# Kernel optimization log

Measured on AMD Instinct MI355X. Metric: run time of the kernel, lower is better.

## Reference

```python
import jax, jax.numpy as jnp
import numpy as np

RESOLUTION = 64
EPS = 1e-08


def setup_inputs() -> dict:
    key = jax.random.key(0)
    k1, k2 = jax.random.split(key)
    pts = jax.random.uniform(k1, (8, 3, 65536), dtype=jnp.float32)
    feat = jax.random.normal(k2, (8, 32, 65536), dtype=jnp.float32)
    return {"pts": pts, "feat": feat}


def reference(pts, feat):
    R = RESOLUTION
    B, _, N = pts.shape
    C = feat.shape[1]
    # Voxel index computation is done under no_grad in the original.
    p = jax.lax.stop_gradient(pts)
    p = p - jnp.min(p, axis=2, keepdims=True)  # per-sample, per-axis min shift
    # Global scalar max of per-point L2 norms (over all batches & points).
    norm_max = jnp.max(jnp.linalg.norm(p, axis=1))
    p = p / (norm_max + EPS)
    idx3 = (p * (R - 1)).astype(jnp.int32)  # [B, 3, N], floor via truncation (coords >= 0)
    vox = idx3[:, 0] + idx3[:, 1] * R + idx3[:, 2] * (R * R)  # [B, N] flat voxel ids

    featT = jnp.transpose(feat, (0, 2, 1))  # [B, N, C]

    def per_sample(v, f):
        # scatter-mean of point features into R^3 voxels; empty voxels -> 0
        sums = jax.ops.segment_sum(f, v, num_segments=R ** 3)          # [R^3, C]
        cnt = jax.ops.segment_sum(jnp.ones((v.shape[0],), f.dtype), v,
                                  num_segments=R ** 3)                 # [R^3]
        return sums / jnp.maximum(cnt, 1.0)[:, None]

    voxel = jax.vmap(per_sample)(vox, featT)  # [B, R^3, C]
    return jnp.transpose(voxel, (0, 2, 1)).reshape(B, C, R, R, R)
```

## Files before the change

kernel.cpp:

```cpp
#include <hip/hip_runtime.h>

#define RES 64
#define R3  (RES*RES*RES)
#define BB  8
#define CC  32
#define NN  65536
#define NBINS (BB*R3)
#define NPTS  (BB*NN)
#define NORM_EPS 1e-8f

#define SCAN_BLK 1024
#define NBLK (NBINS/SCAN_BLK)

#define OFF_COUNTS  4096
#define OFF_OFFSETS (OFF_COUNTS  + NBINS*4)
#define OFF_TOTALS  (OFF_OFFSETS + NBINS*4)
#define OFF_VOX     (OFF_TOTALS  + 65536)
#define OFF_ORDER   (OFF_VOX     + NPTS*4)
#define OFF_FEATT   (OFF_ORDER   + NPTS*4)

__global__ __launch_bounds__(1024) void k_min(const float* __restrict__ pts, float* __restrict__ mins) {
    int ba = blockIdx.x;
    const float* p = pts + (size_t)ba * NN;
    float m = 1e30f;
    for (int i = threadIdx.x; i < NN; i += 1024) m = fminf(m, p[i]);
    __shared__ float red[1024];
    red[threadIdx.x] = m; __syncthreads();
    for (int s = 512; s > 0; s >>= 1) {
        if (threadIdx.x < s) red[threadIdx.x] = fminf(red[threadIdx.x], red[threadIdx.x + s]);
        __syncthreads();
    }
    if (threadIdx.x == 0) mins[ba] = red[0];
}

__global__ void k_normmax(const float* __restrict__ pts, const float* __restrict__ mins,
                          unsigned* __restrict__ nm) {
    int i = blockIdx.x * blockDim.x + threadIdx.x;
    int b = i >> 16, n = i & (NN - 1);
    const float* p = pts + (size_t)b * 3 * NN + n;
    float x = __fsub_rn(p[0],        mins[b*3+0]);
    float y = __fsub_rn(p[NN],       mins[b*3+1]);
    float z = __fsub_rn(p[2*NN],     mins[b*3+2]);
    float s = __fadd_rn(__fadd_rn(__fmul_rn(x, x), __fmul_rn(y, y)), __fmul_rn(z, z));
    float m = __fsqrt_rn(s);
    __shared__ float red[256];
    red[threadIdx.x] = m; __syncthreads();
    for (int st = 128; st > 0; st >>= 1) {
        if (threadIdx.x < st) red[threadIdx.x] = fmaxf(red[threadIdx.x], red[threadIdx.x + st]);
        __syncthreads();
    }
    if (threadIdx.x == 0) atomicMax(nm, __float_as_uint(red[0]));
}

__global__ void k_transpose(const float* __restrict__ feat, float* __restrict__ featT) {
    __shared__ float tile[32][33];
    int blk = blockIdx.x;
    int b  = blk >> 11;
    int n0 = (blk & 2047) << 5;
    int tx = threadIdx.x & 31, ty = threadIdx.x >> 5;
    const float* src = feat + (size_t)b * CC * NN;
    #pragma unroll
    for (int cc = 0; cc < 32; cc += 8)
        tile[cc + ty][tx] = src[(size_t)(cc + ty) * NN + n0 + tx];
    __syncthreads();
    float* dst = featT + ((size_t)b * NN + n0) * CC;
    #pragma unroll
    for (int nn = 0; nn < 32; nn += 8)
        dst[(size_t)(nn + ty) * CC + tx] = tile[tx][nn + ty];
}

__global__ void k_voxid(const float* __restrict__ pts, const float* __restrict__ mins,
                        const unsigned* __restrict__ nm,
                        unsigned* __restrict__ voxid, unsigned* __restrict__ counts) {
    int i = blockIdx.x * blockDim.x + threadIdx.x;
    int b = i >> 16, n = i & (NN - 1);
    float denom = __fadd_rn(__uint_as_float(*nm), NORM_EPS);
    float inv = __fdiv_rn(1.0f, denom);
    const float* p = pts + (size_t)b * 3 * NN + n;
    float x = __fsub_rn(p[0],    mins[b*3+0]);
    float y = __fsub_rn(p[NN],   mins[b*3+1]);
    float z = __fsub_rn(p[2*NN], mins[b*3+2]);
    int ix = (int)(__fmul_rn(__fmul_rn(x, inv), 63.0f));
    int iy = (int)(__fmul_rn(__fmul_rn(y, inv), 63.0f));
    int iz = (int)(__fmul_rn(__fmul_rn(z, inv), 63.0f));
    ix = min(max(ix, 0), RES - 1);
    iy = min(max(iy, 0), RES - 1);
    iz = min(max(iz, 0), RES - 1);
    unsigned vox = (unsigned)(ix + iy * RES + iz * RES * RES);
    voxid[i] = vox;
    atomicAdd(&counts[(size_t)b * R3 + vox], 1u);
}

__global__ void k_scansum(const unsigned* __restrict__ counts, unsigned* __restrict__ totals) {
    int blk = blockIdx.x, t = threadIdx.x;
    const unsigned* p = counts + (size_t)blk * SCAN_BLK;
    unsigned s = 0;
    #pragma unroll
    for (int j = 0; j < 4; j++) s += p[t + 256 * j];
    __shared__ unsigned red[256];
    red[t] = s; __syncthreads();
    for (int st = 128; st > 0; st >>= 1) {
        if (t < st) red[t] += red[t + st];
        __syncthreads();
    }
    if (t == 0) totals[blk] = red[0];
}

__global__ void k_scantop(unsigned* __restrict__ totals) {
    __shared__ unsigned red[256];
    int t = threadIdx.x;
    unsigned v[8], s = 0;
    #pragma unroll
    for (int j = 0; j < 8; j++) { v[j] = totals[t * 8 + j]; s += v[j]; }
    red[t] = s; __syncthreads();
    for (int st = 1; st < 256; st <<= 1) {
        unsigned tmp = (t >= st) ? red[t - st] : 0u;
        __syncthreads();
        red[t] += tmp;
        __syncthreads();
    }
    unsigned acc = (t == 0) ? 0u : red[t - 1];
    #pragma unroll
    for (int j = 0; j < 8; j++) { totals[t * 8 + j] = acc; acc += v[j]; }
}

__global__ void k_scanfinal(const unsigned* __restrict__ counts,
                            const unsigned* __restrict__ totals,
                            unsigned* __restrict__ offsets) {
    __shared__ unsigned red[256];
    int blk = blockIdx.x, t = threadIdx.x;
    const unsigned* p = counts + (size_t)blk * SCAN_BLK;
    unsigned v[4], s = 0;
    #pragma unroll
    for (int j = 0; j < 4; j++) { v[j] = p[t * 4 + j]; s += v[j]; }
    red[t] = s; __syncthreads();
    for (int st = 1; st < 256; st <<= 1) {
        unsigned tmp = (t >= st) ? red[t - st] : 0u;
        __syncthreads();
        red[t] += tmp;
        __syncthreads();
    }
    unsigned acc = totals[blk] + ((t == 0) ? 0u : red[t - 1]);
    unsigned* q = offsets + (size_t)blk * SCAN_BLK;
    #pragma unroll
    for (int j = 0; j < 4; j++) { q[t * 4 + j] = acc; acc += v[j]; }
}

__global__ void k_fill(const unsigned* __restrict__ voxid, unsigned* __restrict__ offsets,
                       unsigned* __restrict__ order) {
    int i = blockIdx.x * blockDim.x + threadIdx.x;
    int b = i >> 16;
    unsigned bin = (unsigned)b * R3 + voxid[i];
    unsigned pos = atomicAdd(&offsets[bin], 1u);
    order[pos] = (unsigned)i;
}

__global__ __launch_bounds__(256) void k_accum(
        const unsigned* __restrict__ counts, const unsigned* __restrict__ offsets,
        const unsigned* __restrict__ order, const float* __restrict__ featT,
        float* __restrict__ out) {
    __shared__ float tile[CC][260];
    int tid = threadIdx.x;
    int bin0 = blockIdx.x << 8;
    int bin  = bin0 + tid;
    int b    = bin >> 18;
    unsigned cnt   = counts[bin];
    unsigned end   = offsets[bin];
    unsigned start = end - cnt;
    float acc[CC];
    #pragma unroll
    for (int c = 0; c < CC; c++) acc[c] = 0.f;
    for (unsigned k = start; k < end; k++) {
        unsigned i = order[k];
        const float4* ft = (const float4*)(featT + (size_t)i * CC);
        #pragma unroll
        for (int q = 0; q < CC / 4; q++) {
            float4 v = ft[q];
            acc[q*4+0] += v.x; acc[q*4+1] += v.y; acc[q*4+2] += v.z; acc[q*4+3] += v.w;
        }
    }
    float inv = __fdiv_rn(1.0f, fmaxf((float)cnt, 1.0f));
    #pragma unroll
    for (int c = 0; c < CC; c++) tile[c][tid] = __fmul_rn(acc[c], inv);
    __syncthreads();
    int vox0 = bin0 & (R3 - 1);
    float* ob = out + (size_t)b * CC * R3 + vox0;
    int lane64 = tid & 63;
    int crow   = tid >> 6;
    #pragma unroll
    for (int cc = 0; cc < CC; cc += 4) {
        int c = cc + crow;
        float4 v = make_float4(tile[c][lane64*4+0], tile[c][lane64*4+1],
                               tile[c][lane64*4+2], tile[c][lane64*4+3]);
        *(float4*)(ob + (size_t)c * R3 + lane64*4) = v;
    }
}

extern "C" void kernel_launch(void* const* d_in, const int* in_sizes, int n_in,
                              void* d_out, int out_size, void* d_ws, size_t ws_size,
                              hipStream_t stream) {
    const float* pts  = (const float*)d_in[0];
    const float* feat = (const float*)d_in[1];
    float* out = (float*)d_out;

    char* ws = (char*)d_ws;
    unsigned* nm      = (unsigned*)ws;
    float*    mins    = (float*)ws + 16;
    unsigned* counts  = (unsigned*)(ws + OFF_COUNTS);
    unsigned* offsets = (unsigned*)(ws + OFF_OFFSETS);
    unsigned* totals  = (unsigned*)(ws + OFF_TOTALS);
    unsigned* voxid   = (unsigned*)(ws + OFF_VOX);
    unsigned* order   = (unsigned*)(ws + OFF_ORDER);
    float*    featT   = (float*)(ws + OFF_FEATT);

    hipMemsetAsync(d_ws, 0, OFF_COUNTS + (size_t)NBINS * 4, stream);

    k_min      <<<BB * 3,           1024, 0, stream>>>(pts, mins);
    k_normmax  <<<NPTS / 256,       256,  0, stream>>>(pts, mins, nm);
    k_transpose<<<BB * (NN / 32),   256,  0, stream>>>(feat, featT);
    k_voxid    <<<NPTS / 256,       256,  0, stream>>>(pts, mins, nm, voxid, counts);
    k_scansum  <<<NBLK,             256,  0, stream>>>(counts, totals);
    k_scantop  <<<1,                256,  0, stream>>>(totals);
    k_scanfinal<<<NBLK,             256,  0, stream>>>(counts, totals, offsets);
    k_fill     <<<NPTS / 256,       256,  0, stream>>>(voxid, offsets, order);
    k_accum    <<<NBINS / 256,      256,  0, stream>>>(counts, offsets, order, featT, out);
}
```

Before: 479.0 us.

## Replace three-pass scan with atomic per-batch segment allocation; vectorize transpose

The global exclusive scan over bin counts (reduce, top scan, final scan) is replaced by a single kernel that scans each 1024-bin chunk locally and reserves a contiguous range within its batch's point region using an atomic cursor. Bins stay contiguous inside a chunk but chunks land in arbitrary order within the batch, which is fine because accumulation only needs start and end per bin. This removes two launches and a pass over the counts array. The feature transpose also switches to float4 loads and stores to cut memory instructions. The cursor sits in the memset region and is zeroed each call.

```diff
diff --git a/kernel.cpp b/kernel.cpp
--- a/kernel.cpp
+++ b/kernel.cpp
@@ -9,13 +9,12 @@
 #define NPTS  (BB*NN)
 #define NORM_EPS 1e-8f
 
-#define SCAN_BLK 1024
-#define NBLK (NBINS/SCAN_BLK)
+#define ALLOC_BINS 1024
+#define NALLOC (NBINS/ALLOC_BINS)
 
 #define OFF_COUNTS  4096
 #define OFF_OFFSETS (OFF_COUNTS  + NBINS*4)
-#define OFF_TOTALS  (OFF_OFFSETS + NBINS*4)
-#define OFF_VOX     (OFF_TOTALS  + 65536)
+#define OFF_VOX     (OFF_OFFSETS + NBINS*4)
 #define OFF_ORDER   (OFF_VOX     + NPTS*4)
 #define OFF_FEATT   (OFF_ORDER   + NPTS*4)
 
@@ -57,16 +56,18 @@
     int blk = blockIdx.x;
     int b  = blk >> 11;
     int n0 = (blk & 2047) << 5;
-    int tx = threadIdx.x & 31, ty = threadIdx.x >> 5;
-    const float* src = feat + (size_t)b * CC * NN;
-    #pragma unroll
-    for (int cc = 0; cc < 32; cc += 8)
-        tile[cc + ty][tx] = src[(size_t)(cc + ty) * NN + n0 + tx];
+    int t = threadIdx.x;
+    int c  = t >> 3;
+    int nq = t & 7;
+    float4 v = *(const float4*)(feat + ((size_t)b * CC + c) * NN + n0 + nq * 4);
+    tile[c][nq*4+0] = v.x; tile[c][nq*4+1] = v.y;
+    tile[c][nq*4+2] = v.z; tile[c][nq*4+3] = v.w;
     __syncthreads();
-    float* dst = featT + ((size_t)b * NN + n0) * CC;
-    #pragma unroll
-    for (int nn = 0; nn < 32; nn += 8)
-        dst[(size_t)(nn + ty) * CC + tx] = tile[tx][nn + ty];
+    int n  = t >> 3;
+    int cq = t & 7;
+    float4 w = make_float4(tile[cq*4+0][n], tile[cq*4+1][n],
+                           tile[cq*4+2][n], tile[cq*4+3][n]);
+    *(float4*)(featT + ((size_t)b * NN + n0 + n) * CC + cq * 4) = w;
 }
 
 __global__ void k_voxid(const float* __restrict__ pts, const float* __restrict__ mins,
@@ -91,45 +92,14 @@
     atomicAdd(&counts[(size_t)b * R3 + vox], 1u);
 }
 
-__global__ void k_scansum(const unsigned* __restrict__ counts, unsigned* __restrict__ totals) {
+__global__ __launch_bounds__(256) void k_alloc(const unsigned* __restrict__ counts,
+                                               unsigned* __restrict__ offsets,
+                                               unsigned* __restrict__ cursor) {
+    __shared__ unsigned red[256];
+    __shared__ unsigned base;
     int blk = blockIdx.x, t = threadIdx.x;
-    const unsigned* p = counts + (size_t)blk * SCAN_BLK;
-    unsigned s = 0;
-    #pragma unroll
-    for (int j = 0; j < 4; j++) s += p[t + 256 * j];
-    __shared__ unsigned red[256];
-    red[t] = s; __syncthreads();
-    for (int st = 128; st > 0; st >>= 1) {
-        if (t < st) red[t] += red[t + st];
-        __syncthreads();
-    }
-    if (t == 0) totals[blk] = red[0];
-}
-
-__global__ void k_scantop(unsigned* __restrict__ totals) {
-    __shared__ unsigned red[256];
-    int t = threadIdx.x;
-    unsigned v[8], s = 0;
-    #pragma unroll
-    for (int j = 0; j < 8; j++) { v[j] = totals[t * 8 + j]; s += v[j]; }
-    red[t] = s; __syncthreads();
-    for (int st = 1; st < 256; st <<= 1) {
-        unsigned tmp = (t >= st) ? red[t - st] : 0u;
-        __syncthreads();
-        red[t] += tmp;
-        __syncthreads();
-    }
-    unsigned acc = (t == 0) ? 0u : red[t - 1];
-    #pragma unroll
-    for (int j = 0; j < 8; j++) { totals[t * 8 + j] = acc; acc += v[j]; }
-}
-
-__global__ void k_scanfinal(const unsigned* __restrict__ counts,
-                            const unsigned* __restrict__ totals,
-                            unsigned* __restrict__ offsets) {
-    __shared__ unsigned red[256];
-    int blk = blockIdx.x, t = threadIdx.x;
-    const unsigned* p = counts + (size_t)blk * SCAN_BLK;
+    int b = blk >> 8;
+    const unsigned* p = counts + (size_t)blk * ALLOC_BINS;
     unsigned v[4], s = 0;
     #pragma unroll
     for (int j = 0; j < 4; j++) { v[j] = p[t * 4 + j]; s += v[j]; }
@@ -140,8 +110,10 @@
         red[t] += tmp;
         __syncthreads();
     }
-    unsigned acc = totals[blk] + ((t == 0) ? 0u : red[t - 1]);
-    unsigned* q = offsets + (size_t)blk * SCAN_BLK;
+    if (t == 255) base = atomicAdd(&cursor[b], red[255]);
+    __syncthreads();
+    unsigned acc = ((unsigned)b << 16) + base + red[t] - s;
+    unsigned* q = offsets + (size_t)blk * ALLOC_BINS;
     #pragma unroll
     for (int j = 0; j < 4; j++) { q[t * 4 + j] = acc; acc += v[j]; }
 }
@@ -150,7 +122,7 @@
                        unsigned* __restrict__ order) {
     int i = blockIdx.x * blockDim.x + threadIdx.x;
     int b = i >> 16;
-    unsigned bin = (unsigned)b * R3 + voxid[i];
+    unsigned bin = ((unsigned)b << 18) + voxid[i];
     unsigned pos = atomicAdd(&offsets[bin], 1u);
     order[pos] = (unsigned)i;
 }
@@ -206,9 +178,9 @@
     char* ws = (char*)d_ws;
     unsigned* nm      = (unsigned*)ws;
     float*    mins    = (float*)ws + 16;
+    unsigned* cursor  = (unsigned*)ws + 64;
     unsigned* counts  = (unsigned*)(ws + OFF_COUNTS);
     unsigned* offsets = (unsigned*)(ws + OFF_OFFSETS);
-    unsigned* totals  = (unsigned*)(ws + OFF_TOTALS);
     unsigned* voxid   = (unsigned*)(ws + OFF_VOX);
     unsigned* order   = (unsigned*)(ws + OFF_ORDER);
     float*    featT   = (float*)(ws + OFF_FEATT);
@@ -219,9 +191,7 @@
     k_normmax  <<<NPTS / 256,       256,  0, stream>>>(pts, mins, nm);
     k_transpose<<<BB * (NN / 32),   256,  0, stream>>>(feat, featT);
     k_voxid    <<<NPTS / 256,       256,  0, stream>>>(pts, mins, nm, voxid, counts);
-    k_scansum  <<<NBLK,             256,  0, stream>>>(counts, totals);
-    k_scantop  <<<1,                256,  0, stream>>>(totals);
-    k_scanfinal<<<NBLK,             256,  0, stream>>>(counts, totals, offsets);
+    k_alloc    <<<NALLOC,           256,  0, stream>>>(counts, offsets, cursor);
     k_fill     <<<NPTS / 256,       256,  0, stream>>>(voxid, offsets, order);
     k_accum    <<<NBINS / 256,      256,  0, stream>>>(counts, offsets, order, featT, out);
 }
```

After: 491.1 us. 1.03x slower.
